# Kernel tuning notes

Hardware: AMD Instinct MI355X
Metric: run time of the kernel (lower is better)

## Reference

```python
import jax, jax.numpy as jnp
import numpy as np

B, S, D = 1, 2048, 1024
H, DK = 16, 64
DFF, E, K = 4096, 8, 2
EPS = float(np.finfo(np.float32).eps)  # torch nn.RMSNorm default eps = finfo.eps


def setup_inputs() -> dict:
    key = jax.random.key(0)
    ks = jax.random.split(key, 8)
    s = 0.02
    return {
        "x": jax.random.normal(ks[0], (B, S, D), jnp.float32),
        "qkv_w": jax.random.normal(ks[1], (3 * D, D), jnp.float32) * s,
        "out_w": jax.random.normal(ks[2], (D, D), jnp.float32) * s,
        "router_w": jax.random.normal(ks[3], (E, D), jnp.float32) * s,
        "w1": jax.random.normal(ks[4], (E, DFF, D), jnp.float32) * s,
        "w2": jax.random.normal(ks[5], (E, D, DFF), jnp.float32) * s,
        "norm1_w": jnp.ones((D,), jnp.float32),
        "norm2_w": jnp.ones((D,), jnp.float32),
    }


def _rmsnorm(x, w):
    return x * jax.lax.rsqrt(jnp.mean(x * x, axis=-1, keepdims=True) + EPS) * w


def _rope(x):
    # x: [B, S, H, dk]; rotate-half RoPE as in RotaryPositionalEmbedding
    dk = x.shape[-1]
    inv_freq = 1.0 / (10000.0 ** (jnp.arange(0, dk, 2, dtype=jnp.float32) / dk))
    t = jnp.arange(x.shape[1], dtype=jnp.float32)
    freqs = t[:, None] * inv_freq[None, :]          # [S, dk/2]
    cos = jnp.cos(freqs)[None, :, None, :]
    sin = jnp.sin(freqs)[None, :, None, :]
    x1, x2 = jnp.split(x, 2, axis=-1)
    return jnp.concatenate([x1 * cos - x2 * sin, x2 * cos + x1 * sin], axis=-1)


def _block(x, qkv_w, out_w, router_w, w1, w2, norm1_w, norm2_w):
    Bv, Sv, Dv = x.shape
    # --- attention with RoPE (causal, eval mode) ---
    h = _rmsnorm(x, norm1_w)
    qkv = (h @ qkv_w.T).reshape(Bv, Sv, 3, H, DK)
    q, k, v = qkv[:, :, 0], qkv[:, :, 1], qkv[:, :, 2]   # [B,S,H,dk]
    q = _rope(q)
    k = _rope(k)
    scores = jnp.einsum('bshd,bthd->bhst', q, k) / np.float32(np.sqrt(DK))
    causal = jnp.tril(jnp.ones((Sv, Sv), dtype=bool))
    scores = jnp.where(causal, scores, jnp.float32(-jnp.inf))
    attn = jax.nn.softmax(scores, axis=-1)
    o = jnp.einsum('bhst,bthd->bshd', attn, v).reshape(Bv, Sv, Dv)
    x = x + o @ out_w.T
    # --- MoE with top-k routing ---
    h2 = _rmsnorm(x, norm2_w).reshape(-1, Dv)            # [T, D]
    logits = h2 @ router_w.T                             # [T, E]
    probs = jax.nn.softmax(logits, axis=-1)
    top_p, top_i = jax.lax.top_k(probs, K)               # [T, K]
    top_p = top_p / jnp.sum(top_p, axis=-1, keepdims=True)
    T = h2.shape[0]
    # dense per-token per-expert combine weights (same math as masked loop)
    w_dense = jnp.zeros((T, E), h2.dtype).at[jnp.arange(T)[:, None], top_i].add(top_p)
    hid = jax.nn.gelu(jnp.einsum('td,efd->etf', h2, w1), approximate=False)  # [E,T,DFF]
    eo = jnp.einsum('etf,edf->etd', hid, w2)                                  # [E,T,D]
    moe = jnp.einsum('etd,te->td', eo, w_dense).reshape(Bv, Sv, Dv)
    aux_loss = E * jnp.sum(jnp.mean(probs, axis=0) ** 2)
    return x + moe, aux_loss


def reference(x, qkv_w, out_w, router_w, w1, w2, norm1_w, norm2_w):
    return _block(x, qkv_w, out_w, router_w, w1, w2, norm1_w, norm2_w)
```

## Files before the change

kernel.cpp:

```cpp
#include <hip/hip_runtime.h>
#include <cstdint>
#include <math.h>

typedef float f32x4 __attribute__((ext_vector_type(4)));
typedef __bf16 bf16x8 __attribute__((ext_vector_type(8)));
typedef unsigned short us4 __attribute__((ext_vector_type(4)));
typedef unsigned short us8 __attribute__((ext_vector_type(8)));

#define DEV static __device__ __forceinline__

DEV unsigned short f2bf(float f){
  union { __bf16 h; unsigned short u; } cv; cv.h = (__bf16)f; return cv.u;
}
DEV float bf2f(unsigned short u){ return __uint_as_float((unsigned int)u << 16); }

DEV void gload16(const void* g, void* l){
  __builtin_amdgcn_global_load_lds((__attribute__((address_space(1))) void*)g,
                                   (__attribute__((address_space(3))) void*)l, 16, 0, 0);
}

__global__ __launch_bounds__(256) void conv_kernel(const float* __restrict__ src,
    unsigned short* __restrict__ dst, int n8){
  int i = blockIdx.x*256 + threadIdx.x;
  if (i >= n8) return;
  float4 a = ((const float4*)src)[2*i];
  float4 b = ((const float4*)src)[2*i+1];
  us8 o = { f2bf(a.x), f2bf(a.y), f2bf(a.z), f2bf(a.w),
            f2bf(b.x), f2bf(b.y), f2bf(b.z), f2bf(b.w) };
  ((us8*)dst)[i] = o;
}

__global__ __launch_bounds__(256) void vtrans_kernel(const unsigned short* __restrict__ qkvb,
    unsigned short* __restrict__ vt){
  int tt = blockIdx.x, h = blockIdx.y;
  int t0 = tt*64;
  __shared__ unsigned short tile[64][72];
  int r = threadIdx.x >> 2, cb = (threadIdx.x & 3) * 16;
  const unsigned short* src = qkvb + (long long)(t0+r)*3072 + 2048 + h*64 + cb;
  us8 a = *(const us8*)src;
  us8 b = *(const us8*)(src+8);
  #pragma unroll
  for (int i=0;i<8;++i){ tile[r][cb+i] = a[i]; tile[r][cb+8+i] = b[i]; }
  __syncthreads();
  unsigned short o[16];
  #pragma unroll
  for (int i=0;i<16;++i) o[i] = tile[cb+i][r];
  unsigned short* dst = vt + (long long)(h*64+r)*2048 + t0 + cb;
  *(us8*)dst = *(us8*)&o[0];
  *(us8*)(dst+8) = *(us8*)&o[8];
}

__global__ __launch_bounds__(256) void rmsnorm_kernel(const float* __restrict__ x, const float* __restrict__ w,
    unsigned short* __restrict__ ob){
  int t = blockIdx.x, tid = threadIdx.x;
  float4 xv = *(const float4*)(x + (long long)t*1024 + tid*4);
  float ss = xv.x*xv.x + xv.y*xv.y + xv.z*xv.z + xv.w*xv.w;
  for (int m=32;m;m>>=1) ss += __shfl_xor(ss,m);
  __shared__ float lds[4];
  if ((tid&63)==0) lds[tid>>6] = ss;
  __syncthreads();
  float tot = lds[0]+lds[1]+lds[2]+lds[3];
  float inv = rsqrtf(tot*(1.0f/1024.0f) + 1.1920928955078125e-07f);
  float4 wv = *(const float4*)(w + tid*4);
  us4 rb = { f2bf(xv.x*inv*wv.x), f2bf(xv.y*inv*wv.y), f2bf(xv.z*inv*wv.z), f2bf(xv.w*inv*wv.w) };
  *(us4*)&ob[(long long)t*1024 + tid*4] = rb;
}

__global__ __launch_bounds__(256) void rmsnorm2_kernel(const float* __restrict__ xp, int ksn, long long kstride,
    const float* __restrict__ w, const float* __restrict__ rw,
    float* __restrict__ x1, unsigned short* __restrict__ hb,
    float* __restrict__ probs, int* __restrict__ tope, float* __restrict__ topw, int* __restrict__ counts){
  int t = blockIdx.x, tid = threadIdx.x;
  long long b = (long long)t*1024 + tid*4;
  float4 xv = {0.f,0.f,0.f,0.f};
  for (int ks=0; ks<ksn; ++ks){
    float4 a = *(const float4*)(xp + ks*kstride + b);
    xv.x+=a.x; xv.y+=a.y; xv.z+=a.z; xv.w+=a.w;
  }
  *(float4*)(x1 + b) = xv;
  float ss = xv.x*xv.x + xv.y*xv.y + xv.z*xv.z + xv.w*xv.w;
  for (int m=32;m;m>>=1) ss += __shfl_xor(ss,m);
  __shared__ float lds[32];
  if ((tid&63)==0) lds[tid>>6] = ss;
  __syncthreads();
  float tot = lds[0]+lds[1]+lds[2]+lds[3];
  float inv = rsqrtf(tot*(1.0f/1024.0f) + 1.1920928955078125e-07f);
  float4 wv = *(const float4*)(w + tid*4);
  float r0 = xv.x*inv*wv.x, r1 = xv.y*inv*wv.y, r2 = xv.z*inv*wv.z, r3 = xv.w*inv*wv.w;
  us4 rb = { f2bf(r0), f2bf(r1), f2bf(r2), f2bf(r3) };
  *(us4*)&hb[b] = rb;
  float pe[8];
  #pragma unroll
  for (int e2=0;e2<8;++e2){
    float4 rv = *(const float4*)(rw + e2*1024 + tid*4);
    pe[e2] = r0*rv.x + r1*rv.y + r2*rv.z + r3*rv.w;
  }
  __syncthreads();
  #pragma unroll
  for (int e2=0;e2<8;++e2){
    float v = pe[e2];
    for (int m=32;m;m>>=1) v += __shfl_xor(v,m);
    if ((tid&63)==0) lds[(tid>>6)*8+e2] = v;
  }
  __syncthreads();
  if (tid==0){
    float lg[8], pp[8];
    #pragma unroll
    for (int e2=0;e2<8;++e2) lg[e2] = lds[e2]+lds[8+e2]+lds[16+e2]+lds[24+e2];
    float mx = lg[0];
    for (int e2=1;e2<8;++e2) mx = fmaxf(mx, lg[e2]);
    float s = 0.f;
    for (int e2=0;e2<8;++e2){ pp[e2] = __expf(lg[e2]-mx); s += pp[e2]; }
    float invs = 1.0f/s;
    int i0 = 0;
    for (int e2=1;e2<8;++e2) if (pp[e2] > pp[i0]) i0 = e2;
    int i1 = (i0==0)?1:0;
    for (int e2=0;e2<8;++e2) if (e2!=i0 && pp[e2] > pp[i1]) i1 = e2;
    for (int e2=0;e2<8;++e2) probs[t*8+e2] = pp[e2]*invs;
    float p0 = pp[i0], p1 = pp[i1], wsum = p0+p1;
    tope[t*2] = i0; tope[t*2+1] = i1;
    topw[t*2] = p0/wsum; topw[t*2+1] = p1/wsum;
    atomicAdd(&counts[i0],1); atomicAdd(&counts[i1],1);
  }
}

template<int EPI, bool GATHER, int BN>
__global__ __launch_bounds__(256) void gemm_bb(
    const unsigned short* __restrict__ A, int lda,
    const unsigned short* __restrict__ Bb, long long bstride, int ldb,
    int M, int N, int K, int KS, long long ksoff,
    const int* __restrict__ counts, const int* __restrict__ offs,
    const int* __restrict__ tok_list, const float* __restrict__ wgt,
    const float* __restrict__ resid,
    float* __restrict__ Cf, unsigned short* __restrict__ Cb, int ldc)
{
  constexpr int MF = (BN==128) ? 4 : 2;
  constexpr int BLOADS = BN/32;
  const int z = blockIdx.z;
  const int e = z / KS, ks = z - e*KS;
  const int Me = counts ? counts[e] : M;
  const int by = blockIdx.y;
  if (by * 128 >= Me) return;
  const int rbase = offs ? offs[e] : 0;
  const int bx = blockIdx.x;
  const unsigned short* B = Bb + (long long)e * bstride;
  const int kn = K / KS;
  const int kbeg = ks * kn;

  __shared__ __align__(16) unsigned short As[128*64];
  __shared__ __align__(16) unsigned short Bs[BN*64];

  const int tid = threadIdx.x, lane = tid & 63, w = tid >> 6;
  const int wr = (BN==128) ? (w >> 1) : w;
  const int wc = (BN==128) ? (w & 1) : 0;
  const int l15 = lane & 15, l4 = lane >> 4;

  const unsigned short* asrc[4];
  #pragma unroll
  for (int j=0;j<4;++j){
    int G = j*256 + tid;
    int R = G >> 3, c = G & 7;
    int sc = c ^ (R & 7);
    int lr = by*128 + R; if (lr >= Me) lr = Me-1;
    int li = rbase + lr;
    int ar = GATHER ? (tok_list[li] >> 1) : li;
    asrc[j] = A + (long long)ar*lda + kbeg + sc*8;
  }
  const unsigned short* bsrc[BLOADS];
  #pragma unroll
  for (int j=0;j<BLOADS;++j){
    int G = j*256 + tid;
    int R = G >> 3, c = G & 7;
    int sc = c ^ (R & 7);
    bsrc[j] = B + (long long)(bx*BN + R)*ldb + kbeg + sc*8;
  }

  f32x4 acc[MF][4] = {};

  for (int k0 = 0; k0 < kn; k0 += 64){
    __syncthreads();
    #pragma unroll
    for (int j=0;j<4;++j) gload16(asrc[j] + k0, &As[(j*256+tid)*8]);
    #pragma unroll
    for (int j=0;j<BLOADS;++j) gload16(bsrc[j] + k0, &Bs[(j*256+tid)*8]);
    __syncthreads();
    #pragma unroll
    for (int kk=0;kk<2;++kk){
      bf16x8 af[MF], bfr[4];
      #pragma unroll
      for (int m=0;m<MF;++m){
        int R = wr*(MF*16) + m*16 + l15;
        int c = (l4 + 4*kk) ^ (R&7);
        af[m] = *(const bf16x8*)&As[R*64 + c*8];
      }
      #pragma unroll
      for (int n=0;n<4;++n){
        int R = wc*64 + n*16 + l15;
        int c = (l4 + 4*kk) ^ (R&7);
        bfr[n] = *(const bf16x8*)&Bs[R*64 + c*8];
      }
      #pragma unroll
      for (int m=0;m<MF;++m)
        #pragma unroll
        for (int n=0;n<4;++n)
          acc[m][n] = __builtin_amdgcn_mfma_f32_16x16x32_bf16(af[m], bfr[n], acc[m][n], 0, 0, 0);
    }
  }

  #pragma unroll
  for (int m=0;m<MF;++m){
    #pragma unroll
    for (int r2=0;r2<4;++r2){
      int lr = by*128 + wr*(MF*16) + m*16 + 4*l4 + r2;
      if (lr >= Me) continue;
      #pragma unroll
      for (int n=0;n<4;++n){
        int col = bx*BN + wc*64 + n*16 + l15;
        float v = acc[m][n][r2];
        if constexpr (EPI == 1){
          if (ks == 0) v += resid[(long long)lr*ldc + col];
          Cf[ks*ksoff + (long long)lr*ldc + col] = v;
        } else if constexpr (EPI == 2){
          float g = 0.5f * v * (1.0f + erff(v * 0.70710678118654752f));
          Cb[(long long)(rbase+lr)*ldc + col] = f2bf(g);
        } else if constexpr (EPI == 3){
          int gi = rbase + lr;
          int ts = tok_list[gi];
          Cf[ks*ksoff + (long long)ts*ldc + col] = v * wgt[gi];
        } else {
          Cb[(long long)lr*ldc + col] = f2bf(v);
        }
      }
    }
  }
}

__global__ __launch_bounds__(256) void rope_kernel(const unsigned short* __restrict__ qkvb,
    unsigned short* __restrict__ q, unsigned short* __restrict__ k){
  int t = blockIdx.x, tid = threadIdx.x;
  const unsigned short* row = qkvb + (long long)t*3072;
  #pragma unroll
  for (int u2=0; u2<2; ++u2){
    int pid = tid + u2*256;
    int hh = pid >> 5, j = pid & 31;
    float invf = __expf(-(float)j * 0.28782313662425575f);
    float fr = (float)t * invf;
    float sn, cs;
    __sincosf(fr, &sn, &cs);
    int base = hh*64 + j;
    long long ob_ = (long long)t*1024 + base;
    float a = bf2f(row[base]), b = bf2f(row[base+32]);
    q[ob_]    = f2bf(a*cs - b*sn);
    q[ob_+32] = f2bf(b*cs + a*sn);
    a = bf2f(row[1024+base]); b = bf2f(row[1024+base+32]);
    k[ob_]    = f2bf(a*cs - b*sn);
    k[ob_+32] = f2bf(b*cs + a*sn);
  }
}

__global__ __launch_bounds__(256) void attn_kernel(
    const unsigned short* __restrict__ Q,
    const unsigned short* __restrict__ K,
    const unsigned short* __restrict__ Vt,
    unsigned short* __restrict__ O)
{
  const int bx = gridDim.x - 1 - blockIdx.x;
  const int h = blockIdx.y;
  const int q0 = bx*64;
  const int tid = threadIdx.x, lane = tid&63, w = tid>>6;
  const int l15 = lane & 15, l4 = lane >> 4;

  __shared__ __align__(16) unsigned short Ks[64*64];
  __shared__ __align__(16) unsigned short Vs[64*64];
  __shared__ __align__(16) unsigned short Ps[4*16*64];
  unsigned short* Pw = Ps + w*1024;

  const int qrow = q0 + w*16 + l15;
  bf16x8 aq[2];
  #pragma unroll
  for (int kk=0;kk<2;++kk)
    aq[kk] = *(const bf16x8*)&Q[(long long)qrow*1024 + h*64 + 32*kk + 8*l4];

  f32x4 o[4] = {};
  float Mx[4] = {-INFINITY,-INFINITY,-INFINITY,-INFINITY};
  float Ls[4] = {0.f,0.f,0.f,0.f};

  const int row_g = q0 + w*16 + 4*l4;
  const int nt = bx + 1;
  for (int it = 0; it < nt; ++it){
    int k0 = it*64;
    #pragma unroll
    for (int i=0;i<2;++i){
      int seg = 4*i + w;
      int row = seg*8 + (lane>>3);
      int cs = (lane&7) ^ (row&7);
      gload16(&K[(long long)(k0+row)*1024 + h*64 + cs*8], &Ks[seg*512]);
      gload16(&Vt[(long long)(h*64+row)*2048 + k0 + cs*8], &Vs[seg*512]);
    }
    __syncthreads();
    f32x4 st[4];
    #pragma unroll
    for (int kt=0;kt<4;++kt){
      f32x4 s = {0.f,0.f,0.f,0.f};
      #pragma unroll
      for (int kk=0;kk<2;++kk){
        int R = kt*16 + l15;
        int ch = (l4+4*kk) ^ (R&7);
        bf16x8 bk = *(const bf16x8*)&Ks[R*64 + ch*8];
        s = __builtin_amdgcn_mfma_f32_16x16x32_bf16(aq[kk], bk, s, 0,0,0);
      }
      st[kt] = s;
    }
    #pragma unroll
    for (int kt=0;kt<4;++kt){
      int col = k0 + kt*16 + l15;
      #pragma unroll
      for (int r=0;r<4;++r){
        float vv = st[kt][r]*0.125f;
        st[kt][r] = (col <= row_g + r) ? vv : -INFINITY;
      }
    }
    float sf[4];
    #pragma unroll
    for (int r=0;r<4;++r){
      float mx = fmaxf(fmaxf(st[0][r],st[1][r]),fmaxf(st[2][r],st[3][r]));
      mx = fmaxf(mx, __shfl_xor(mx,1));
      mx = fmaxf(mx, __shfl_xor(mx,2));
      mx = fmaxf(mx, __shfl_xor(mx,4));
      mx = fmaxf(mx, __shfl_xor(mx,8));
      float mn = fmaxf(Mx[r], mx);
      float sc = __expf(Mx[r]-mn);
      Mx[r]=mn; sf[r]=sc;
      float ls=0.f;
      #pragma unroll
      for (int kt=0;kt<4;++kt){ float pp = __expf(st[kt][r]-mn); st[kt][r]=pp; ls+=pp; }
      Ls[r] = Ls[r]*sc + ls;
    }
    #pragma unroll
    for (int dt=0;dt<4;++dt)
      #pragma unroll
      for (int r=0;r<4;++r) o[dt][r] *= sf[r];
    #pragma unroll
    for (int kt=0;kt<4;++kt)
      #pragma unroll
      for (int r=0;r<4;++r){
        int prow = 4*l4+r, pcol = kt*16+l15;
        int byteoff = (prow*128 + pcol*2) ^ ((prow&7)<<4);
        *(unsigned short*)((char*)Pw + byteoff) = f2bf(st[kt][r]);
      }
    bf16x8 pa[2];
    #pragma unroll
    for (int kk=0;kk<2;++kk){
      int pr = l15;
      int ch = (l4+4*kk) ^ (pr&7);
      pa[kk] = *(const bf16x8*)&Pw[pr*64 + ch*8];
    }
    #pragma unroll
    for (int dt=0;dt<4;++dt){
      #pragma unroll
      for (int kk=0;kk<2;++kk){
        int R = dt*16 + l15;
        int c = (l4 + 4*kk) ^ (R&7);
        bf16x8 bv = *(const bf16x8*)&Vs[R*64 + c*8];
        o[dt] = __builtin_amdgcn_mfma_f32_16x16x32_bf16(pa[kk], bv, o[dt], 0,0,0);
      }
    }
    __syncthreads();
  }
  #pragma unroll
  for (int r=0;r<4;++r){
    float l = Ls[r];
    l += __shfl_xor(l,1); l += __shfl_xor(l,2); l += __shfl_xor(l,4); l += __shfl_xor(l,8);
    Ls[r] = 1.0f / l;
  }
  #pragma unroll
  for (int dt=0;dt<4;++dt)
    #pragma unroll
    for (int r=0;r<4;++r){
      float vv = o[dt][r]*Ls[r];
      int rg = row_g + r;
      O[(long long)rg*1024 + h*64 + dt*16 + l15] = f2bf(vv);
    }
}

__global__ void init_kernel(int* counts, int* cursor){
  int i = threadIdx.x;
  if (i<8){ counts[i]=0; cursor[i]=0; }
}

__global__ void prefix_kernel(const int* counts, int* offs){
  if (threadIdx.x==0){
    int a=0;
    for (int e2=0;e2<8;++e2){ offs[e2]=a; a+=counts[e2]; }
  }
}

__global__ void scatter_kernel(const int* __restrict__ tope, const float* __restrict__ topw,
    const int* __restrict__ offs, int* __restrict__ cursor, int* __restrict__ tok_list, float* __restrict__ wgt){
  int t = blockIdx.x*blockDim.x + threadIdx.x;
  if (t >= 2048) return;
  #pragma unroll
  for (int s=0;s<2;++s){
    int e2 = tope[t*2+s];
    int pos = atomicAdd(&cursor[e2], 1);
    int i = offs[e2] + pos;
    tok_list[i] = t*2+s;
    wgt[i] = topw[t*2+s];
  }
}

__global__ __launch_bounds__(256) void aux_kernel(const float* __restrict__ probs, float* __restrict__ out){
  int tid = threadIdx.x;
  float pe[8] = {0,0,0,0,0,0,0,0};
  for (int t = tid; t < 2048; t += 256){
    #pragma unroll
    for (int e2=0;e2<8;++e2) pe[e2] += probs[t*8+e2];
  }
  __shared__ float lds[32];
  #pragma unroll
  for (int e2=0;e2<8;++e2){
    float v = pe[e2];
    for (int m=32;m;m>>=1) v += __shfl_xor(v,m);
    if ((tid&63)==0) lds[(tid>>6)*8 + e2] = v;
  }
  __syncthreads();
  if (tid==0){
    float aux = 0.f;
    #pragma unroll
    for (int e2=0;e2<8;++e2){
      float mean = (lds[e2]+lds[8+e2]+lds[16+e2]+lds[24+e2]) * (1.0f/2048.0f);
      aux += mean*mean;
    }
    out[2097152] = 8.0f * aux;
  }
}

__global__ __launch_bounds__(256) void final_kernel(const float* __restrict__ x1, const float* __restrict__ slots,
    int ksn, long long kstride, float* __restrict__ out){
  int t = blockIdx.x, tid = threadIdx.x;
  long long b = (long long)t*1024 + tid*4;
  float4 a = *(const float4*)(x1 + b);
  long long s = (long long)t*2048 + tid*4;
  for (int ks=0; ks<ksn; ++ks){
    float4 s0 = *(const float4*)(slots + ks*kstride + s);
    float4 s1 = *(const float4*)(slots + ks*kstride + s + 1024);
    a.x += s0.x + s1.x; a.y += s0.y + s1.y; a.z += s0.z + s1.z; a.w += s0.w + s1.w;
  }
  *(float4*)(out + b) = a;
}

extern "C" void kernel_launch(void* const* d_in, const int* in_sizes, int n_in,
                              void* d_out, int out_size, void* d_ws, size_t ws_size,
                              hipStream_t stream)
{
  (void)in_sizes; (void)n_in; (void)out_size; (void)ws_size;
  const float* x    = (const float*)d_in[0];
  const float* qkvw = (const float*)d_in[1];
  const float* outw = (const float*)d_in[2];
  const float* rw   = (const float*)d_in[3];
  const float* w1   = (const float*)d_in[4];
  const float* w2   = (const float*)d_in[5];
  const float* n1w  = (const float*)d_in[6];
  const float* n2w  = (const float*)d_in[7];
  float* out = (float*)d_out;

  char* base = (char*)d_ws;
  const size_t MB = 1ull<<20;
  const int KSO = 4;
  const int KSW = 2;

  unsigned short* h_b  = (unsigned short*)(base + 0*MB);
  unsigned short* qb   = (unsigned short*)(base + 4*MB);
  unsigned short* kb   = (unsigned short*)(base + 8*MB);
  unsigned short* ob   = (unsigned short*)(base + 12*MB);
  unsigned short* qkvb = (unsigned short*)(base + 16*MB);
  unsigned short* vt   = (unsigned short*)(base + 28*MB);
  unsigned short* hid  = (unsigned short*)(base + 0*MB);

  unsigned short* wbq = (unsigned short*)(base + 32*MB);
  unsigned short* wbo = (unsigned short*)(base + 40*MB);
  unsigned short* wb  = (unsigned short*)(base + 32*MB);

  float* x1p   = (float*)(base + 96*MB);
  float* slots = (float*)(base + 96*MB);
  float* x1    = (float*)(base + 136*MB);
  unsigned short* h2b = (unsigned short*)(base + 144*MB);
  char* small_ = base + 148*MB;

  float* probs = (float*)(small_);
  int*   tope  = (int*)(small_ + 256*1024);
  float* topw  = (float*)(small_ + 512*1024);
  int*   tok_list = (int*)(small_ + 768*1024);
  float* wgt   = (float*)(small_ + 1024*1024);
  int*   counts= (int*)(small_ + 1536*1024);
  int*   offs  = (int*)(small_ + 1536*1024 + 256);
  int*   cursor= (int*)(small_ + 1536*1024 + 512);

  init_kernel<<<1,64,0,stream>>>(counts, cursor);
  rmsnorm_kernel<<<2048,256,0,stream>>>(x, n1w, h_b);
  conv_kernel<<<1536,256,0,stream>>>(qkvw, wbq, 3*1024*1024/8);
  conv_kernel<<<512,256,0,stream>>>(outw, wbo, 1024*1024/8);
  gemm_bb<4,false,64><<<dim3(48,16,1),256,0,stream>>>(h_b,1024, wbq,0,1024, 2048,3072,1024, 1,0,
      nullptr,nullptr,nullptr,nullptr,nullptr, nullptr,qkvb,3072);
  rope_kernel<<<2048,256,0,stream>>>(qkvb, qb, kb);
  vtrans_kernel<<<dim3(32,16),256,0,stream>>>(qkvb, vt);
  attn_kernel<<<dim3(32,16),256,0,stream>>>(qb, kb, vt, ob);
  gemm_bb<1,false,64><<<dim3(16,16,KSO),256,0,stream>>>(ob,1024, wbo,0,1024, 2048,1024,1024, KSO,(long long)2048*1024,
      nullptr,nullptr,nullptr,nullptr, x, x1p,nullptr,1024);
  rmsnorm2_kernel<<<2048,256,0,stream>>>(x1p, KSO, (long long)2048*1024, n2w, rw, x1, h2b,
      probs, tope, topw, counts);
  prefix_kernel<<<1,64,0,stream>>>(counts, offs);
  scatter_kernel<<<8,256,0,stream>>>(tope, topw, offs, cursor, tok_list, wgt);
  conv_kernel<<<16384,256,0,stream>>>(w1, wb, 32*1024*1024/8);
  gemm_bb<2,true,128><<<dim3(32,16,8),256,0,stream>>>(h2b,1024, wb,(long long)4096*1024,1024, 2048,4096,1024, 1,0,
      counts,offs,tok_list,nullptr,nullptr, nullptr,hid,4096);
  conv_kernel<<<16384,256,0,stream>>>(w2, wb, 32*1024*1024/8);
  gemm_bb<3,false,128><<<dim3(8,16,8*KSW),256,0,stream>>>(hid,4096, wb,(long long)4096*1024,4096, 2048,1024,4096, KSW,(long long)4096*1024,
      counts,offs,tok_list,wgt,nullptr, slots,nullptr,1024);
  aux_kernel<<<1,256,0,stream>>>(probs, out);
  final_kernel<<<2048,256,0,stream>>>(x1, slots, KSW, (long long)4096*1024, out);
}
```

Measured before the change: 402.3 us.

## Fuse RoPE into QKV GEMM epilogue, store MoE slots in bf16, merge aux kernel

Applies RoPE directly in the QKV GEMM epilogue and writes Q and K in rotated form, with V going to a separate compact buffer. This removes the rope kernel and the round trip of the full QKV tensor. The MoE down-projection now writes weighted slot outputs as bf16 instead of fp32, which halves slot traffic but costs accuracy. The aux-loss reduction moves into block 0 of the final kernel, saving one launch.

```diff
diff --git a/kernel.cpp b/kernel.cpp
--- a/kernel.cpp
+++ b/kernel.cpp
@@ -30,13 +30,13 @@
   ((us8*)dst)[i] = o;
 }
 
-__global__ __launch_bounds__(256) void vtrans_kernel(const unsigned short* __restrict__ qkvb,
+__global__ __launch_bounds__(256) void vtrans_kernel(const unsigned short* __restrict__ vb,
     unsigned short* __restrict__ vt){
   int tt = blockIdx.x, h = blockIdx.y;
   int t0 = tt*64;
   __shared__ unsigned short tile[64][72];
   int r = threadIdx.x >> 2, cb = (threadIdx.x & 3) * 16;
-  const unsigned short* src = qkvb + (long long)(t0+r)*3072 + 2048 + h*64 + cb;
+  const unsigned short* src = vb + (long long)(t0+r)*1024 + h*64 + cb;
   us8 a = *(const us8*)src;
   us8 b = *(const us8*)(src+8);
   #pragma unroll
@@ -132,7 +132,8 @@
     const int* __restrict__ counts, const int* __restrict__ offs,
     const int* __restrict__ tok_list, const float* __restrict__ wgt,
     const float* __restrict__ resid,
-    float* __restrict__ Cf, unsigned short* __restrict__ Cb, int ldc)
+    float* __restrict__ Cf, unsigned short* __restrict__ Cb, int ldc,
+    unsigned short* __restrict__ Q2, unsigned short* __restrict__ K2)
 {
   constexpr int MF = (BN==128) ? 4 : 2;
   constexpr int BLOADS = BN/32;
@@ -207,6 +208,36 @@
     }
   }
 
+  if constexpr (EPI == 6){
+    #pragma unroll
+    for (int m=0;m<MF;++m){
+      #pragma unroll
+      for (int r2=0;r2<4;++r2){
+        int lr = by*128 + wr*(MF*16) + m*16 + 4*l4 + r2;
+        if (bx < 32){
+          unsigned short* dst = (bx < 16) ? Q2 : K2;
+          int h = bx & 15;
+          #pragma unroll
+          for (int n=0;n<2;++n){
+            int j = n*16 + l15;
+            float invf = __expf(-(float)j * 0.28782313662425575f);
+            float sn, cs;
+            __sincosf((float)lr * invf, &sn, &cs);
+            float a = acc[m][n][r2], b2 = acc[m][n+2][r2];
+            dst[(long long)lr*1024 + h*64 + j]      = f2bf(a*cs - b2*sn);
+            dst[(long long)lr*1024 + h*64 + j + 32] = f2bf(b2*cs + a*sn);
+          }
+        } else {
+          int vcol = (bx-32)*64;
+          #pragma unroll
+          for (int n=0;n<4;++n)
+            Cb[(long long)lr*1024 + vcol + n*16 + l15] = f2bf(acc[m][n][r2]);
+        }
+      }
+    }
+    return;
+  }
+
   #pragma unroll
   for (int m=0;m<MF;++m){
     #pragma unroll
@@ -227,34 +258,15 @@
           int gi = rbase + lr;
           int ts = tok_list[gi];
           Cf[ks*ksoff + (long long)ts*ldc + col] = v * wgt[gi];
+        } else if constexpr (EPI == 5){
+          int gi = rbase + lr;
+          int ts = tok_list[gi];
+          Cb[ks*ksoff + (long long)ts*ldc + col] = f2bf(v * wgt[gi]);
         } else {
           Cb[(long long)lr*ldc + col] = f2bf(v);
         }
       }
     }
-  }
-}
-
-__global__ __launch_bounds__(256) void rope_kernel(const unsigned short* __restrict__ qkvb,
-    unsigned short* __restrict__ q, unsigned short* __restrict__ k){
-  int t = blockIdx.x, tid = threadIdx.x;
-  const unsigned short* row = qkvb + (long long)t*3072;
-  #pragma unroll
-  for (int u2=0; u2<2; ++u2){
-    int pid = tid + u2*256;
-    int hh = pid >> 5, j = pid & 31;
-    float invf = __expf(-(float)j * 0.28782313662425575f);
-    float fr = (float)t * invf;
-    float sn, cs;
-    __sincosf(fr, &sn, &cs);
-    int base = hh*64 + j;
-    long long ob_ = (long long)t*1024 + base;
-    float a = bf2f(row[base]), b = bf2f(row[base+32]);
-    q[ob_]    = f2bf(a*cs - b*sn);
-    q[ob_+32] = f2bf(b*cs + a*sn);
-    a = bf2f(row[1024+base]); b = bf2f(row[1024+base+32]);
-    k[ob_]    = f2bf(a*cs - b*sn);
-    k[ob_+32] = f2bf(b*cs + a*sn);
   }
 }
 
@@ -409,44 +421,46 @@
   }
 }
 
-__global__ __launch_bounds__(256) void aux_kernel(const float* __restrict__ probs, float* __restrict__ out){
-  int tid = threadIdx.x;
-  float pe[8] = {0,0,0,0,0,0,0,0};
-  for (int t = tid; t < 2048; t += 256){
-    #pragma unroll
-    for (int e2=0;e2<8;++e2) pe[e2] += probs[t*8+e2];
-  }
-  __shared__ float lds[32];
-  #pragma unroll
-  for (int e2=0;e2<8;++e2){
-    float v = pe[e2];
-    for (int m=32;m;m>>=1) v += __shfl_xor(v,m);
-    if ((tid&63)==0) lds[(tid>>6)*8 + e2] = v;
-  }
-  __syncthreads();
-  if (tid==0){
-    float aux = 0.f;
-    #pragma unroll
-    for (int e2=0;e2<8;++e2){
-      float mean = (lds[e2]+lds[8+e2]+lds[16+e2]+lds[24+e2]) * (1.0f/2048.0f);
-      aux += mean*mean;
-    }
-    out[2097152] = 8.0f * aux;
-  }
-}
-
-__global__ __launch_bounds__(256) void final_kernel(const float* __restrict__ x1, const float* __restrict__ slots,
-    int ksn, long long kstride, float* __restrict__ out){
+__global__ __launch_bounds__(256) void final_kernel(const float* __restrict__ x1,
+    const unsigned short* __restrict__ slots, int ksn, long long kstride,
+    const float* __restrict__ probs, float* __restrict__ out){
   int t = blockIdx.x, tid = threadIdx.x;
   long long b = (long long)t*1024 + tid*4;
   float4 a = *(const float4*)(x1 + b);
   long long s = (long long)t*2048 + tid*4;
   for (int ks=0; ks<ksn; ++ks){
-    float4 s0 = *(const float4*)(slots + ks*kstride + s);
-    float4 s1 = *(const float4*)(slots + ks*kstride + s + 1024);
-    a.x += s0.x + s1.x; a.y += s0.y + s1.y; a.z += s0.z + s1.z; a.w += s0.w + s1.w;
+    us4 s0 = *(const us4*)(slots + ks*kstride + s);
+    us4 s1 = *(const us4*)(slots + ks*kstride + s + 1024);
+    a.x += bf2f(s0[0]) + bf2f(s1[0]);
+    a.y += bf2f(s0[1]) + bf2f(s1[1]);
+    a.z += bf2f(s0[2]) + bf2f(s1[2]);
+    a.w += bf2f(s0[3]) + bf2f(s1[3]);
   }
   *(float4*)(out + b) = a;
+  if (blockIdx.x == 0){
+    float pe[8] = {0,0,0,0,0,0,0,0};
+    for (int tt = tid; tt < 2048; tt += 256){
+      #pragma unroll
+      for (int e2=0;e2<8;++e2) pe[e2] += probs[tt*8+e2];
+    }
+    __shared__ float lds[32];
+    #pragma unroll
+    for (int e2=0;e2<8;++e2){
+      float v = pe[e2];
+      for (int m=32;m;m>>=1) v += __shfl_xor(v,m);
+      if ((tid&63)==0) lds[(tid>>6)*8 + e2] = v;
+    }
+    __syncthreads();
+    if (tid==0){
+      float aux = 0.f;
+      #pragma unroll
+      for (int e2=0;e2<8;++e2){
+        float mean = (lds[e2]+lds[8+e2]+lds[16+e2]+lds[24+e2]) * (1.0f/2048.0f);
+        aux += mean*mean;
+      }
+      out[2097152] = 8.0f * aux;
+    }
+  }
 }
 
 extern "C" void kernel_launch(void* const* d_in, const int* in_sizes, int n_in,
@@ -473,7 +487,7 @@
   unsigned short* qb   = (unsigned short*)(base + 4*MB);
   unsigned short* kb   = (unsigned short*)(base + 8*MB);
   unsigned short* ob   = (unsigned short*)(base + 12*MB);
-  unsigned short* qkvb = (unsigned short*)(base + 16*MB);
+  unsigned short* vb   = (unsigned short*)(base + 16*MB);
   unsigned short* vt   = (unsigned short*)(base + 28*MB);
   unsigned short* hid  = (unsigned short*)(base + 0*MB);
 
@@ -482,7 +496,7 @@
   unsigned short* wb  = (unsigned short*)(base + 32*MB);
 
   float* x1p   = (float*)(base + 96*MB);
-  float* slots = (float*)(base + 96*MB);
+  unsigned short* slots_b = (unsigned short*)(base + 96*MB);
   float* x1    = (float*)(base + 136*MB);
   unsigned short* h2b = (unsigned short*)(base + 144*MB);
   char* small_ = base + 148*MB;
@@ -500,23 +514,21 @@
   rmsnorm_kernel<<<2048,256,0,stream>>>(x, n1w, h_b);
   conv_kernel<<<1536,256,0,stream>>>(qkvw, wbq, 3*1024*1024/8);
   conv_kernel<<<512,256,0,stream>>>(outw, wbo, 1024*1024/8);
-  gemm_bb<4,false,64><<<dim3(48,16,1),256,0,stream>>>(h_b,1024, wbq,0,1024, 2048,3072,1024, 1,0,
-      nullptr,nullptr,nullptr,nullptr,nullptr, nullptr,qkvb,3072);
-  rope_kernel<<<2048,256,0,stream>>>(qkvb, qb, kb);
-  vtrans_kernel<<<dim3(32,16),256,0,stream>>>(qkvb, vt);
+  gemm_bb<6,false,64><<<dim3(48,16,1),256,0,stream>>>(h_b,1024, wbq,0,1024, 2048,3072,1024, 1,0,
+      nullptr,nullptr,nullptr,nullptr,nullptr, nullptr,vb,3072, qb,kb);
+  vtrans_kernel<<<dim3(32,16),256,0,stream>>>(vb, vt);
   attn_kernel<<<dim3(32,16),256,0,stream>>>(qb, kb, vt, ob);
   gemm_bb<1,false,64><<<dim3(16,16,KSO),256,0,stream>>>(ob,1024, wbo,0,1024, 2048,1024,1024, KSO,(long long)2048*1024,
-      nullptr,nullptr,nullptr,nullptr, x, x1p,nullptr,1024);
+      nullptr,nullptr,nullptr,nullptr, x, x1p,nullptr,1024, nullptr,nullptr);
   rmsnorm2_kernel<<<2048,256,0,stream>>>(x1p, KSO, (long long)2048*1024, n2w, rw, x1, h2b,
       probs, tope, topw, counts);
   prefix_kernel<<<1,64,0,stream>>>(counts, offs);
   scatter_kernel<<<8,256,0,stream>>>(tope, topw, offs, cursor, tok_list, wgt);
   conv_kernel<<<16384,256,0,stream>>>(w1, wb, 32*1024*1024/8);
   gemm_bb<2,true,128><<<dim3(32,16,8),256,0,stream>>>(h2b,1024, wb,(long long)4096*1024,1024, 2048,4096,1024, 1,0,
-      counts,offs,tok_list,nullptr,nullptr, nullptr,hid,4096);
+      counts,offs,tok_list,nullptr,nullptr, nullptr,hid,4096, nullptr,nullptr);
   conv_kernel<<<16384,256,0,stream>>>(w2, wb, 32*1024*1024/8);
-  gemm_bb<3,false,128><<<dim3(8,16,8*KSW),256,0,stream>>>(hid,4096, wb,(long long)4096*1024,4096, 2048,1024,4096, KSW,(long long)4096*1024,
-      counts,offs,tok_list,wgt,nullptr, slots,nullptr,1024);
-  aux_kernel<<<1,256,0,stream>>>(probs, out);
-  final_kernel<<<2048,256,0,stream>>>(x1, slots, KSW, (long long)4096*1024, out);
-}
+  gemm_bb<5,false,128><<<dim3(8,16,8*KSW),256,0,stream>>>(hid,4096, wb,(long long)4096*1024,4096, 2048,1024,4096, KSW,(long long)4096*1024,
+      counts,offs,tok_list,wgt,nullptr, nullptr,slots_b,1024, nullptr,nullptr);
+  final_kernel<<<2048,256,0,stream>>>(x1, slots_b, KSW, (long long)4096*1024, probs, out);
+}
```

New measurement: 394.4 us (median of 2 runs). -2.0%, faster.
